# Performance work log

Hardware: AMD Instinct MI355X
Metric: run time of the kernel (lower is better)

## Reference

```python
import jax, jax.numpy as jnp
import numpy as np
from jax import lax

B, T, L = 256, 1024, 64


def setup_inputs() -> dict:
    key = jax.random.key(0)
    k1, k2, k3, k4 = jax.random.split(key, 4)
    logits = jax.random.normal(k1, (B, T, L), dtype=jnp.float32)
    labels = jax.random.randint(k2, (B, T), 0, L, dtype=jnp.int32)
    seq_lens = jax.random.randint(k3, (B,), 1, T + 1, dtype=jnp.int32)
    trans = jax.random.uniform(k4, (L, L), dtype=jnp.float32)
    return {"logits": logits, "labels": labels, "seq_lens": seq_lens, "trans": trans}


def _crf_neg_log_likelihood_sum(logits, trans, labels, seq_lens):
    # logits: [B,T,L], trans: [L,L], labels: [B,T] int, seq_lens: [B] int
    b, t, l = logits.shape
    pos = jnp.arange(t)
    mask = pos[None, :] < seq_lens[:, None]          # [B,T] valid tokens
    maskf = mask.astype(logits.dtype)

    # --- sequence score (numerator) ---
    unary = jnp.take_along_axis(logits, labels[..., None], axis=2)[..., 0]  # [B,T]
    unary_score = jnp.sum(unary * maskf, axis=1)                             # [B]
    pair = trans[labels[:, :-1], labels[:, 1:]]                              # [B,T-1]
    pair_maskf = (pos[None, 1:] < seq_lens[:, None]).astype(logits.dtype)    # t+1 valid
    binary_score = jnp.sum(pair * pair_maskf, axis=1)                        # [B]
    seq_score = unary_score + binary_score

    # --- forward algorithm (log partition) ---
    alpha0 = logits[:, 0, :]                                                 # [B,L]
    logits_t = jnp.swapaxes(logits, 0, 1)[1:]                                # [T-1,B,L]
    valid_t = jnp.swapaxes(mask, 0, 1)[1:]                                   # [T-1,B]

    def step(alpha, xs):
        logit, valid = xs                                                    # [B,L],[B]
        # logsumexp over previous tag: alpha[b,i] + trans[i,j]
        new = jax.nn.logsumexp(alpha[:, :, None] + trans[None, :, :], axis=1) + logit
        alpha = jnp.where(valid[:, None], new, alpha)
        return alpha, None

    alpha, _ = lax.scan(step, alpha0, (logits_t, valid_t))
    log_norm = jax.nn.logsumexp(alpha, axis=-1)                              # [B]

    log_likelihood = seq_score - log_norm
    return jnp.sum(-log_likelihood)


def reference(logits, labels, seq_lens, trans):
    return _crf_neg_log_likelihood_sum(logits, trans, labels, seq_lens)
```

## Files before the change

### kernel.cpp

```cpp
#include <hip/hip_runtime.h>

#define TT 1024
#define LL 64
#define BB 256
#define WARM 4
#define NWAVES 4096
#define LOG2E 1.44269504088896340736f
#define LN2   0.69314718055994530942f

typedef __fp16 h2 __attribute__((ext_vector_type(2)));
typedef int    i4 __attribute__((ext_vector_type(4)));
__device__ __forceinline__ h2  i2h(int x) { union { int i; h2 h; } u; u.i = x; return u.h; }
__device__ __forceinline__ int h2i(h2 x)  { union { int i; h2 h; } u; u.h = x; return u.i; }


__global__ __launch_bounds__(256) void crf_prefix_kernel(
    const int* __restrict__ seq_lens, int* __restrict__ meta)
{
    __shared__ int sbuf[BB];
    const int tid = threadIdx.x;
    int wv = 0;
    if (tid < BB) { int sl = seq_lens[tid]; wv = (sl > 1) ? (sl - 1) : 1; }
    sbuf[tid] = wv;
    __syncthreads();
    for (int off = 1; off < BB; off <<= 1) {
        int v = (tid >= off) ? sbuf[tid - off] : 0;
        __syncthreads();
        sbuf[tid] += v;
        __syncthreads();
    }
    meta[tid + 1] = sbuf[tid];
    if (tid == 0) {
        meta[0] = 0;
        int W = sbuf[BB - 1];
        meta[BB + 1] = (W + NWAVES - 1) / NWAVES;
    }
}

__global__ __launch_bounds__(256) void crf_piece_kernel(
    const float* __restrict__ logits,
    const int*   __restrict__ labels,
    const int*   __restrict__ seq_lens,
    const float* __restrict__ trans,
    const int*   __restrict__ meta,
    float*       __restrict__ part)
{
    __shared__ __align__(16) int shq[4][32];
    const int wid  = blockIdx.x * 4 + (threadIdx.x >> 6);
    const int lane = threadIdx.x & 63;
    int* const shb = &shq[threadIdx.x >> 6][0];

    int ej[32];
    #pragma unroll
    for (int m = 0; m < 32; ++m) {
        float e0 = __builtin_amdgcn_exp2f(trans[(2 * m)     * LL + lane] * LOG2E);
        float e1 = __builtin_amdgcn_exp2f(trans[(2 * m + 1) * LL + lane] * LOG2E);
        ej[m] = h2i(__builtin_amdgcn_cvt_pkrtz(e0, e1));
    }

    const int W = meta[BB];
    const int K = meta[BB + 1];
    int g0 = wid * K;
    int g1 = g0 + K; g1 = (g1 < W) ? g1 : W;

#define RENORM(V) { \
    int eb_ = (__builtin_amdgcn_readfirstlane(__float_as_int(V)) >> 23) & 0xFF; \
    C += eb_ - 127; \
    float scl_ = __int_as_float((254 - eb_) << 23); \
    u = (V) * scl_; \
}
#define PACKD() { \
    float un_ = __shfl_xor(u, 1, 64); \
    int upk_ = h2i(__builtin_amdgcn_cvt_pkrtz(u, un_)); \
    if (!(lane & 1)) shb[lane >> 1] = upk_; \
    asm volatile("" ::: "memory"); \
}
#define MEAS(OUT) { \
    float us_ = u; \
    _Pragma("unroll") \
    for (int off_ = 32; off_; off_ >>= 1) us_ += __shfl_xor(us_, off_, 64); \
    OUT = ((float)C + __builtin_amdgcn_logf(us_)) * LN2; \
}
#define RS(I) { \
    float g_ = __builtin_amdgcn_exp2f(fR##I * LOG2E); \
    fR##I = lg[ldoff]; \
    ldoff = (ldoff + LL) & (TT * LL - 1); \
    i4 w_[8]; \
    _Pragma("unroll") \
    for (int r_ = 0; r_ < 8; ++r_) \
        __builtin_memcpy(&w_[r_], shb + 4 * r_, 16); \
    float a1_ = 0.f, a2_ = 0.f, a3_ = 0.f, a4_ = 0.f; \
    _Pragma("unroll") \
    for (int r_ = 0; r_ < 8; ++r_) { \
        a1_ = __builtin_amdgcn_fdot2(i2h(w_[r_][0]), i2h(ej[4 * r_]),     a1_, false); \
        a2_ = __builtin_amdgcn_fdot2(i2h(w_[r_][1]), i2h(ej[4 * r_ + 1]), a2_, false); \
        a3_ = __builtin_amdgcn_fdot2(i2h(w_[r_][2]), i2h(ej[4 * r_ + 2]), a3_, false); \
        a4_ = __builtin_amdgcn_fdot2(i2h(w_[r_][3]), i2h(ej[4 * r_ + 3]), a4_, false); \
    } \
    float v_ = ((a1_ + a2_) + (a3_ + a4_)) * g_; \
    RENORM(v_); \
    PACKD(); \
}
#define WS(I, SLOT) { \
    RS(SLOT); \
    if (start + (I) == lo - 1) MEAS(A_in); \
    if (start + (I) == hi - 1) MEAS(A_out); \
}

    float result = 0.f;
    while (g0 < g1) {
        int blo = 0, bhi = BB;
        while (bhi - blo > 1) {
            int mid = (blo + bhi) >> 1;
            if (meta[mid] <= g0) blo = mid; else bhi = mid;
        }
        const int b  = blo;
        const int pe = meta[b + 1];
        const int units = ((g1 < pe) ? g1 : pe) - g0;
        const int lo = g0 - meta[b] + 1;
        const int slen = seq_lens[b];
        const int hi = (lo + units < slen) ? (lo + units) : slen;
        const float* lg  = logits + (size_t)b * TT * LL;
        const int*   lab = labels + b * TT;

        float sc = 0.f;
        for (int t0 = lo + lane; t0 < hi; t0 += 64) {
            int l1 = lab[t0];
            sc += lg[(size_t)t0 * LL + l1] + trans[lab[t0 - 1] * LL + l1];
        }
        if (lo == 1 && lane == 0) sc += lg[lab[0]];
        #pragma unroll
        for (int off = 32; off; off >>= 1) sc += __shfl_xor(sc, off, 64);

        const int start = (lo - WARM > 1) ? (lo - WARM) : 1;
        const int warmN = (lo > 1) ? WARM : 0;
        int C = 0;
        float u;

        u = __builtin_amdgcn_exp2f(lg[lane + (start - 1) * LL] * LOG2E);
        {
            float v0 = u;
            RENORM(v0);
        }
        PACKD();

        unsigned ldoff = (unsigned)(lane + start * LL);
        float fR0 = lg[ldoff]; ldoff += LL;
        float fR1 = lg[ldoff]; ldoff += LL;
        float fR2 = lg[ldoff]; ldoff += LL;
        float fR3 = lg[ldoff]; ldoff += LL;

        float A_in = 0.f, A_out = 0.f;

        if (warmN) {
            WS(0, 0); WS(1, 1); WS(2, 2); WS(3, 3);
        }

        const int n = hi - start - warmN;
        if (n > 0) {
            for (int r = n >> 3; r > 0; --r) {
                RS(0); RS(1); RS(2); RS(3);
                RS(0); RS(1); RS(2); RS(3);
            }
            const int rem = n & 7;
            if (rem > 0) { RS(0);
            if (rem > 1) { RS(1);
            if (rem > 2) { RS(2);
            if (rem > 3) { RS(3);
            if (rem > 4) { RS(0);
            if (rem > 5) { RS(1);
            if (rem > 6) { RS(2); }}}}}}}
            MEAS(A_out);
        } else if (warmN == 0) {
            MEAS(A_out);
        }

        result += (A_out - A_in) - sc;
        g0 += units;
    }

    if (lane == 0) part[wid] = result;
}

__global__ __launch_bounds__(1024) void reduce_kernel(
    const float* __restrict__ part, float* __restrict__ out)
{
    int tid = threadIdx.x;
    float v = 0.f;
    #pragma unroll
    for (int i = 0; i < 4; ++i) v += part[tid + 1024 * i];
    #pragma unroll
    for (int off = 32; off; off >>= 1) v += __shfl_xor(v, off, 64);
    __shared__ float r[16];
    if ((tid & 63) == 0) r[tid >> 6] = v;
    __syncthreads();
    if (tid == 0) {
        float s = 0.f;
        #pragma unroll
        for (int i = 0; i < 16; ++i) s += r[i];
        out[0] = s;
    }
}

extern "C" void kernel_launch(void* const* d_in, const int* in_sizes, int n_in,
                              void* d_out, int out_size, void* d_ws, size_t ws_size,
                              hipStream_t stream) {
    const float* logits   = (const float*)d_in[0];
    const int*   labels   = (const int*)d_in[1];
    const int*   seq_lens = (const int*)d_in[2];
    const float* trans    = (const float*)d_in[3];

    int*   meta = (int*)d_ws;
    float* part = (float*)((char*)d_ws + 4096);

    crf_prefix_kernel<<<1, 256, 0, stream>>>(seq_lens, meta);
    crf_piece_kernel<<<1024, 256, 0, stream>>>(logits, labels, seq_lens, trans,
                                               meta, part);
    reduce_kernel<<<1, 1024, 0, stream>>>(part, (float*)d_out);
}
```

Before: 40.04 us.

## Split the per-step dot product across wave halves and combine with a permlane32 swap

```diff
diff --git a/kernel.cpp b/kernel.cpp
--- a/kernel.cpp
+++ b/kernel.cpp
@@ -10,9 +10,14 @@
 
 typedef __fp16 h2 __attribute__((ext_vector_type(2)));
 typedef int    i4 __attribute__((ext_vector_type(4)));
+typedef unsigned u2v __attribute__((ext_vector_type(2)));
 __device__ __forceinline__ h2  i2h(int x) { union { int i; h2 h; } u; u.i = x; return u.h; }
 __device__ __forceinline__ int h2i(h2 x)  { union { int i; h2 h; } u; u.h = x; return u.i; }
 
+
+#if __has_builtin(__builtin_amdgcn_permlane32_swap)
+#define HAVE_PSWAP 1
+#endif
 
 __global__ __launch_bounds__(256) void crf_prefix_kernel(
     const int* __restrict__ seq_lens, int* __restrict__ meta)
@@ -48,14 +53,21 @@
     __shared__ __align__(16) int shq[4][32];
     const int wid  = blockIdx.x * 4 + (threadIdx.x >> 6);
     const int lane = threadIdx.x & 63;
+    const int h    = lane >> 5;
+    const int k    = lane & 31;
     int* const shb = &shq[threadIdx.x >> 6][0];
-
-    int ej[32];
+    const int hb   = 16 * h;
+
+    int ejX[16], ejY[16];
     #pragma unroll
-    for (int m = 0; m < 32; ++m) {
-        float e0 = __builtin_amdgcn_exp2f(trans[(2 * m)     * LL + lane] * LOG2E);
-        float e1 = __builtin_amdgcn_exp2f(trans[(2 * m + 1) * LL + lane] * LOG2E);
-        ej[m] = h2i(__builtin_amdgcn_cvt_pkrtz(e0, e1));
+    for (int m = 0; m < 16; ++m) {
+        const int i0 = 32 * h + 2 * m;
+        float e00 = __builtin_amdgcn_exp2f(trans[i0 * LL + 2 * k] * LOG2E);
+        float e10 = __builtin_amdgcn_exp2f(trans[(i0 + 1) * LL + 2 * k] * LOG2E);
+        float e01 = __builtin_amdgcn_exp2f(trans[i0 * LL + 2 * k + 1] * LOG2E);
+        float e11 = __builtin_amdgcn_exp2f(trans[(i0 + 1) * LL + 2 * k + 1] * LOG2E);
+        ejX[m] = h2i(__builtin_amdgcn_cvt_pkrtz(e00, e10));
+        ejY[m] = h2i(__builtin_amdgcn_cvt_pkrtz(e01, e11));
     }
 
     const int W = meta[BB];
@@ -63,44 +75,66 @@
     int g0 = wid * K;
     int g1 = g0 + K; g1 = (g1 < W) ? g1 : W;
 
-#define RENORM(V) { \
-    int eb_ = (__builtin_amdgcn_readfirstlane(__float_as_int(V)) >> 23) & 0xFF; \
-    C += eb_ - 127; \
-    float scl_ = __int_as_float((254 - eb_) << 23); \
-    u = (V) * scl_; \
-}
-#define PACKD() { \
-    float un_ = __shfl_xor(u, 1, 64); \
-    int upk_ = h2i(__builtin_amdgcn_cvt_pkrtz(u, un_)); \
-    if (!(lane & 1)) shb[lane >> 1] = upk_; \
+#define RENORM2(V0, V1) { \
+    int eb_ = (__builtin_amdgcn_readfirstlane(__float_as_int(V0)) >> 23) & 0xFF; \
+    C += eb_ - 125; \
+    float scl_ = __int_as_float((252 - eb_) << 23); \
+    u0 = (V0) * scl_; u1 = (V1) * scl_; \
+}
+#define PUBL() { \
+    int upk_ = h2i(__builtin_amdgcn_cvt_pkrtz(u0, u1)); \
+    if (lane < 32) shb[lane] = upk_; \
     asm volatile("" ::: "memory"); \
 }
 #define MEAS(OUT) { \
-    float us_ = u; \
+    float us_ = u0 + u1; \
     _Pragma("unroll") \
     for (int off_ = 32; off_; off_ >>= 1) us_ += __shfl_xor(us_, off_, 64); \
-    OUT = ((float)C + __builtin_amdgcn_logf(us_)) * LN2; \
+    OUT = ((float)C + __builtin_amdgcn_logf(us_) - 1.0f) * LN2; \
 }
 #define RS(I) { \
-    float g_ = __builtin_amdgcn_exp2f(fR##I * LOG2E); \
-    fR##I = lg[ldoff]; \
-    ldoff = (ldoff + LL) & (TT * LL - 1); \
-    i4 w_[8]; \
+    float ga_ = __builtin_amdgcn_exp2f(fR##I.x * LOG2E); \
+    float gb_ = __builtin_amdgcn_exp2f(fR##I.y * LOG2E); \
+    fR##I = lg2[ldoff]; \
+    ldoff = (ldoff + 32) & (TT * 32 - 1); \
+    i4 w_[4]; \
     _Pragma("unroll") \
-    for (int r_ = 0; r_ < 8; ++r_) \
-        __builtin_memcpy(&w_[r_], shb + 4 * r_, 16); \
-    float a1_ = 0.f, a2_ = 0.f, a3_ = 0.f, a4_ = 0.f; \
+    for (int r_ = 0; r_ < 4; ++r_) \
+        __builtin_memcpy(&w_[r_], shb + hb + 4 * r_, 16); \
+    float x0_ = 0.f, x1_ = 0.f, x2_ = 0.f, x3_ = 0.f; \
+    float y0_ = 0.f, y1_ = 0.f, y2_ = 0.f, y3_ = 0.f; \
     _Pragma("unroll") \
-    for (int r_ = 0; r_ < 8; ++r_) { \
-        a1_ = __builtin_amdgcn_fdot2(i2h(w_[r_][0]), i2h(ej[4 * r_]),     a1_, false); \
-        a2_ = __builtin_amdgcn_fdot2(i2h(w_[r_][1]), i2h(ej[4 * r_ + 1]), a2_, false); \
-        a3_ = __builtin_amdgcn_fdot2(i2h(w_[r_][2]), i2h(ej[4 * r_ + 2]), a3_, false); \
-        a4_ = __builtin_amdgcn_fdot2(i2h(w_[r_][3]), i2h(ej[4 * r_ + 3]), a4_, false); \
+    for (int r_ = 0; r_ < 4; ++r_) { \
+        x0_ = __builtin_amdgcn_fdot2(i2h(w_[r_][0]), i2h(ejX[4 * r_]),     x0_, false); \
+        x1_ = __builtin_amdgcn_fdot2(i2h(w_[r_][1]), i2h(ejX[4 * r_ + 1]), x1_, false); \
+        x2_ = __builtin_amdgcn_fdot2(i2h(w_[r_][2]), i2h(ejX[4 * r_ + 2]), x2_, false); \
+        x3_ = __builtin_amdgcn_fdot2(i2h(w_[r_][3]), i2h(ejX[4 * r_ + 3]), x3_, false); \
+        y0_ = __builtin_amdgcn_fdot2(i2h(w_[r_][0]), i2h(ejY[4 * r_]),     y0_, false); \
+        y1_ = __builtin_amdgcn_fdot2(i2h(w_[r_][1]), i2h(ejY[4 * r_ + 1]), y1_, false); \
+        y2_ = __builtin_amdgcn_fdot2(i2h(w_[r_][2]), i2h(ejY[4 * r_ + 2]), y2_, false); \
+        y3_ = __builtin_amdgcn_fdot2(i2h(w_[r_][3]), i2h(ejY[4 * r_ + 3]), y3_, false); \
     } \
-    float v_ = ((a1_ + a2_) + (a3_ + a4_)) * g_; \
-    RENORM(v_); \
-    PACKD(); \
-}
+    float X_ = (x0_ + x1_) + (x2_ + x3_); \
+    float Y_ = (y0_ + y1_) + (y2_ + y3_); \
+    int pk_ = h2i(__builtin_amdgcn_cvt_pkrtz(X_, Y_)); \
+    h2 sp_; \
+    { COMBINE(pk_, sp_); } \
+    float v0_ = (float)sp_[0] * ga_; \
+    float v1_ = (float)sp_[1] * gb_; \
+    RENORM2(v0_, v1_); \
+    PUBL(); \
+}
+#ifdef HAVE_PSWAP
+#define COMBINE(PK, SP) { \
+    u2v sw_ = __builtin_amdgcn_permlane32_swap((unsigned)(PK), (unsigned)(PK), false, false); \
+    SP = i2h((int)sw_[0]) + i2h((int)sw_[1]); \
+}
+#else
+#define COMBINE(PK, SP) { \
+    int q_ = __shfl_xor((PK), 32, 64); \
+    SP = i2h(PK) + i2h(q_); \
+}
+#endif
 #define WS(I, SLOT) { \
     RS(SLOT); \
     if (start + (I) == lo - 1) MEAS(A_in); \
@@ -120,8 +154,9 @@
         const int lo = g0 - meta[b] + 1;
         const int slen = seq_lens[b];
         const int hi = (lo + units < slen) ? (lo + units) : slen;
-        const float* lg  = logits + (size_t)b * TT * LL;
-        const int*   lab = labels + b * TT;
+        const float*  lg  = logits + (size_t)b * TT * LL;
+        const float2* lg2 = (const float2*)lg;
+        const int*    lab = labels + b * TT;
 
         float sc = 0.f;
         for (int t0 = lo + lane; t0 < hi; t0 += 64) {
@@ -135,20 +170,21 @@
         const int start = (lo - WARM > 1) ? (lo - WARM) : 1;
         const int warmN = (lo > 1) ? WARM : 0;
         int C = 0;
-        float u;
-
-        u = __builtin_amdgcn_exp2f(lg[lane + (start - 1) * LL] * LOG2E);
+        float u0, u1;
+
         {
-            float v0 = u;
-            RENORM(v0);
-        }
-        PACKD();
-
-        unsigned ldoff = (unsigned)(lane + start * LL);
-        float fR0 = lg[ldoff]; ldoff += LL;
-        float fR1 = lg[ldoff]; ldoff += LL;
-        float fR2 = lg[ldoff]; ldoff += LL;
-        float fR3 = lg[ldoff]; ldoff += LL;
+            float2 r0 = lg2[k + (start - 1) * 32];
+            float v0 = __builtin_amdgcn_exp2f(r0.x * LOG2E);
+            float v1 = __builtin_amdgcn_exp2f(r0.y * LOG2E);
+            RENORM2(v0, v1);
+        }
+        PUBL();
+
+        unsigned ldoff = (unsigned)(k + start * 32);
+        float2 fR0 = lg2[ldoff]; ldoff += 32;
+        float2 fR1 = lg2[ldoff]; ldoff += 32;
+        float2 fR2 = lg2[ldoff]; ldoff += 32;
+        float2 fR3 = lg2[ldoff]; ldoff += 32;
 
         float A_in = 0.f, A_out = 0.f;
 
```

New measurement: 45.55 us. 13.8% more time.
